# Kernel tuning notes

Measured on AMD Instinct MI355X. Metric: run time of the kernel, lower is better.

## Reference

```python
import jax, jax.numpy as jnp
import numpy as np
from jax import lax

B, T, M = 32, 1024, 40
CONV, H, C = 128, 256, 10
EPS = 1e-5
POOLS = (5, 4, 2)  # mel-axis maxpool sizes; 5*4*2 == n_mels == 40


def setup_inputs() -> dict:
    key = jax.random.key(0)
    ks = jax.random.split(key, 30)
    rn = lambda k, s, sc=0.05: jax.random.normal(k, s, dtype=jnp.float32) * sc
    inp = {}
    inp["features"] = jax.random.normal(ks[0], (B, 1, T, M), dtype=jnp.float32)
    inp["targets"] = (jax.random.uniform(ks[1], (B, T, C)) > 0.5).astype(jnp.float32)
    inp["force_mask"] = jax.random.bernoulli(ks[2], 0.7, (T, B))  # teacher_forcing_prob=0.7
    chans = [(1, CONV), (CONV, CONV), (CONV, CONV)]
    for i, (ci, co) in enumerate(chans, 1):
        inp[f"W{i}"] = rn(ks[3 * i], (co, ci, 5, 5))
        inp[f"b{i}"] = jnp.zeros((co,), jnp.float32)
        inp[f"g{i}"] = jnp.ones((co,), jnp.float32)
        inp[f"be{i}"] = jnp.zeros((co,), jnp.float32)
        inp[f"m{i}"] = rn(ks[3 * i + 1], (co,), 0.01)
        inp[f"v{i}"] = jnp.ones((co,), jnp.float32)
    inp["Wih"] = rn(ks[20], (3 * H, CONV + C))
    inp["Whh"] = rn(ks[21], (3 * H, H))
    inp["bih"] = jnp.zeros((3 * H,), jnp.float32)
    inp["bhh"] = jnp.zeros((3 * H,), jnp.float32)
    inp["Wf"] = rn(ks[22], (C, H))
    inp["bf"] = jnp.zeros((C,), jnp.float32)
    return inp


def _conv_block(x, W, b, g, be, m, v, pool):
    # Conv2d(k=5, s=1, p=2) + BatchNorm2d (inference) + ReLU + MaxPool2d((1,pool))
    y = lax.conv_general_dilated(x, W, window_strides=(1, 1), padding=((2, 2), (2, 2)),
                                 dimension_numbers=("NCHW", "OIHW", "NCHW"))
    y = y + b[None, :, None, None]
    scale = g * lax.rsqrt(v + EPS)
    y = y * scale[None, :, None, None] + (be - m * scale)[None, :, None, None]
    y = jax.nn.relu(y)
    return lax.reduce_window(y, -jnp.inf, lax.max, (1, 1, 1, pool), (1, 1, 1, pool), "VALID")


def _crnn(features, targets, force_mask, W1, b1, g1, be1, m1, v1, W2, b2, g2, be2, m2, v2,
          W3, b3, g3, be3, m3, v3, Wih, Whh, bih, bhh, Wf, bf):
    x = features  # [B,1,T,M]
    for (W, b, g, be, m, v, p) in ((W1, b1, g1, be1, m1, v1, POOLS[0]),
                                   (W2, b2, g2, be2, m2, v2, POOLS[1]),
                                   (W3, b3, g3, be3, m3, v3, POOLS[2])):
        x = _conv_block(x, W, b, g, be, m, v, p)
    feats = jnp.transpose(x[:, :, :, 0], (2, 0, 1))  # mel pooled to 1 -> [T,B,CONV]

    def step(carry, xs):
        h, tf = carry
        xt, tgt_t, ft = xs  # [B,CONV], [B,C], [B]
        inp = jnp.concatenate([xt, tf], axis=-1)  # [B, CONV+C]
        gi = inp @ Wih.T + bih
        gh = h @ Whh.T + bhh
        ir, iz, inn = jnp.split(gi, 3, axis=-1)
        hr, hz, hn = jnp.split(gh, 3, axis=-1)
        r = jax.nn.sigmoid(ir + hr)
        z = jax.nn.sigmoid(iz + hz)
        n = jnp.tanh(inn + r * hn)
        h = (1.0 - z) * n + z * h
        out = h @ Wf.T + bf  # [B,C]
        pred = (jax.nn.sigmoid(out) > 0.5).astype(jnp.float32)
        tf = jnp.where(ft[:, None], tgt_t, pred)  # teacher-forcing select
        return (h, tf), out

    init = (jnp.zeros((B, H), jnp.float32), jnp.zeros((B, C), jnp.float32))
    xs = (feats, jnp.transpose(targets, (1, 0, 2)), force_mask)
    _, outs = lax.scan(step, init, xs)  # [T,B,C]
    return jnp.transpose(outs, (1, 0, 2))  # [B,T,C]


def reference(features, targets, force_mask, W1, b1, g1, be1, m1, v1, W2, b2, g2, be2, m2, v2,
              W3, b3, g3, be3, m3, v3, Wih, Whh, bih, bhh, Wf, bf):
    return _crnn(features, targets, force_mask, W1, b1, g1, be1, m1, v1, W2, b2, g2, be2, m2, v2,
                 W3, b3, g3, be3, m3, v3, Wih, Whh, bih, bhh, Wf, bf)
```

## Files before the change

kernel.cpp:

```cpp
#include <hip/hip_runtime.h>
#include <math.h>

#define EPSF 1e-5f

typedef __attribute__((ext_vector_type(2))) float f2;
typedef __attribute__((ext_vector_type(4))) float f4;
typedef __attribute__((ext_vector_type(8))) _Float16 f16x8;

template<int CTRL>
__device__ __forceinline__ float dpp_add(float v) {
    int s = __builtin_amdgcn_update_dpp(0, __float_as_int(v), CTRL, 0xf, 0xf, true);
    return v + __int_as_float(s);
}

#define HQ(d) ((d) + (((d) >> 4) << 2))

__global__ __launch_bounds__(256) void k_prep(
    const float* __restrict__ Wih, const float* __restrict__ Whh,
    const float* __restrict__ W2, const float* __restrict__ W3,
    const unsigned char* __restrict__ fmask,
    unsigned int* __restrict__ WhhP, float* __restrict__ WxT,
    _Float16* __restrict__ W2F, float* __restrict__ W3T, int* __restrict__ flag)
{
    int idx = blockIdx.x * 256 + threadIdx.x;
    if (idx < 98304) {
        int T = idx >> 8;
        int lane = (idx >> 2) & 63;
        int j = idx & 3;
        int RT = T >> 3, kt = T & 7;
        int row = RT * 16 + (lane & 15);
        int col = kt * 32 + (lane >> 4) * 8 + j * 2;
        union { _Float16 h[2]; unsigned int u; } pk;
        pk.h[0] = (_Float16)Whh[row * 256 + col];
        pk.h[1] = (_Float16)Whh[row * 256 + col + 1];
        WhhP[idx] = pk.u;
    }
    if (idx < 105984) {
        int j = idx / 138, k = idx % 138;
        if (k < 128) WxT[k * 768 + j] = Wih[idx];
    }
    if (idx < 409600) {
        int f = idx & 7, lane = (idx >> 3) & 63, cot = (idx >> 9) & 7;
        int cc = (idx >> 12) & 3, T = idx >> 14;
        int k = cc * 32 + (lane >> 4) * 8 + f;
        int co = cot * 16 + (lane & 15);
        int dt = T / 5, dm = T % 5;
        W2F[idx] = (_Float16)W2[co * 3200 + k * 25 + dt * 5 + dm];
        int co3 = idx / 3200, r = idx % 3200;
        int ci = r / 25, tap = r % 25;
        W3T[(tap * 128 + ci) * 128 + co3] = W3[idx];
    }
    if (idx == 0) {
        int nz = 0;
        for (int i = 0; i < 4096; i++) if ((i & 3) != 0) nz |= fmask[i];
        *flag = nz ? 0 : 1;
    }
}

__global__ __launch_bounds__(256) void k_conv1(
    const float* __restrict__ X, const float* __restrict__ W1,
    const float* __restrict__ bb, const float* __restrict__ gg,
    const float* __restrict__ be, const float* __restrict__ mm_,
    const float* __restrict__ vv, _Float16* __restrict__ X1h,
    _Float16* __restrict__ X1l)
{
    __shared__ __align__(16) float xs[8][44];
    __shared__ __align__(16) float ws[25][128];
    __shared__ float sc[128], sh[128];
    int bid = blockIdx.x;
    int b = bid >> 8, t0 = (bid & 255) << 2;
    int tid = threadIdx.x;
    for (int e = tid; e < 8 * 44; e += 256) {
        int tt = e / 44, mm = e % 44;
        int gt = t0 + tt - 2, gm = mm - 2;
        float val = 0.f;
        if (gt >= 0 && gt < 1024 && gm >= 0 && gm < 40)
            val = X[(b * 1024 + gt) * 40 + gm];
        xs[tt][mm] = val;
    }
    for (int e = tid; e < 3200; e += 256) {
        int tap = e >> 7, co = e & 127;
        ws[tap][co] = W1[co * 25 + tap];
    }
    if (tid < 128) {
        float s = gg[tid] / sqrtf(vv[tid] + EPSF);
        sc[tid] = s;
        sh[tid] = (bb[tid] - mm_[tid]) * s + be[tid];
    }
    __syncthreads();
    int cog = tid >> 5;
    int m1i = (tid >> 2) & 7;
    int tp  = tid & 3;
    int co0 = cog * 16;
    float val[5][16];
#pragma unroll
    for (int p = 0; p < 5; p++)
#pragma unroll
        for (int i = 0; i < 16; i++) val[p][i] = 0.f;
#pragma unroll
    for (int dt = 0; dt < 5; dt++) {
#pragma unroll
        for (int dm = 0; dm < 5; dm++) {
            float w[16];
#pragma unroll
            for (int i = 0; i < 16; i += 4)
                *(float4*)&w[i] = *(const float4*)&ws[dt * 5 + dm][co0 + i];
#pragma unroll
            for (int p = 0; p < 5; p++) {
                float x = xs[tp + dt][m1i * 5 + p + dm];
#pragma unroll
                for (int i = 0; i < 16; i++) val[p][i] = fmaf(x, w[i], val[p][i]);
            }
        }
    }
    f16x8 h0, h1, l0, l1;
#pragma unroll
    for (int i = 0; i < 16; i++) {
        float s = sc[co0 + i], h = sh[co0 + i];
        float mx = 0.f;
#pragma unroll
        for (int p = 0; p < 5; p++) {
            float y = fmaf(val[p][i], s, h);
            y = fmaxf(y, 0.f);
            mx = fmaxf(mx, y);
        }
        _Float16 hh = (_Float16)mx;
        _Float16 ll = (_Float16)(mx - (float)hh);
        if (i < 8) { h0[i] = hh; l0[i] = ll; }
        else       { h1[i - 8] = hh; l1[i - 8] = ll; }
    }
    long off = (((long)(b * 1024 + t0 + tp)) * 8 + m1i) * 128 + co0;
    *(f16x8*)&X1h[off] = h0;
    *(f16x8*)&X1h[off + 8] = h1;
    *(f16x8*)&X1l[off] = l0;
    *(f16x8*)&X1l[off + 8] = l1;
}

__global__ __launch_bounds__(256) void k_conv2(
    const _Float16* __restrict__ X1h, const _Float16* __restrict__ X1l,
    const _Float16* __restrict__ W2F,
    const float* __restrict__ bb, const float* __restrict__ gg,
    const float* __restrict__ be, const float* __restrict__ mm_,
    const float* __restrict__ vv, float* __restrict__ X2)
{
    __shared__ __align__(16) _Float16 xsh[144 * 40];
    __shared__ __align__(16) _Float16 xsl[144 * 40];
    __shared__ float sc[128], sh[128];
    int bid = blockIdx.x;
    int b = bid >> 7, t0 = (bid & 127) << 3;
    int tid = threadIdx.x;
    int wv = tid >> 6, l = tid & 63;
    int rowc = l & 15, ks = (l >> 4) << 3;
    int tloc = rowc >> 3, mloc = rowc & 7;
    if (tid < 128) {
        float s = gg[tid] / sqrtf(vv[tid] + EPSF);
        sc[tid] = s;
        sh[tid] = (bb[tid] - mm_[tid]) * s + be[tid];
    }
    f4 acc[4][2];
#pragma unroll
    for (int Mt = 0; Mt < 4; Mt++) {
        acc[Mt][0] = (f4){0.f, 0.f, 0.f, 0.f};
        acc[Mt][1] = (f4){0.f, 0.f, 0.f, 0.f};
    }

    for (int cc = 0; cc < 4; cc++) {
        __syncthreads();
        for (int e = tid; e < 1152; e += 256) {
            int w2 = (e >= 576) ? 1 : 0;
            int ee = e - 576 * w2;
            int r = ee >> 2, q = ee & 3;
            int tt = r / 12, mm2 = r % 12;
            int gt = t0 + tt - 2, gm = mm2 - 2;
            f16x8 v;
#pragma unroll
            for (int z = 0; z < 8; z++) v[z] = (_Float16)0.f;
            if (gt >= 0 && gt < 1024 && gm >= 0 && gm < 8) {
                const _Float16* src = w2 ? X1l : X1h;
                v = *(const f16x8*)&src[(((long)(b * 1024 + gt)) * 8 + gm) * 128 + cc * 32 + q * 8];
            }
            _Float16* dst = w2 ? xsl : xsh;
            *(f16x8*)&dst[r * 40 + q * 8] = v;
        }
        __syncthreads();
        for (int dt = 0; dt < 5; dt++) {
#pragma unroll
            for (int dm = 0; dm < 5; dm++) {
                const _Float16* wb = &W2F[(((long)((dt * 5 + dm) * 4 + cc) * 8) * 64) * 8];
                f16x8 b0 = *(const f16x8*)&wb[((wv * 2 + 0) * 64 + l) * 8];
                f16x8 b1 = *(const f16x8*)&wb[((wv * 2 + 1) * 64 + l) * 8];
#pragma unroll
                for (int Mt = 0; Mt < 4; Mt++) {
                    int ai = ((Mt * 2 + tloc + dt) * 12 + (mloc + dm)) * 40 + ks;
                    f16x8 ah = *(const f16x8*)&xsh[ai];
                    f16x8 al = *(const f16x8*)&xsl[ai];
                    acc[Mt][0] = __builtin_amdgcn_mfma_f32_16x16x32_f16(ah, b0, acc[Mt][0], 0, 0, 0);
                    acc[Mt][0] = __builtin_amdgcn_mfma_f32_16x16x32_f16(al, b0, acc[Mt][0], 0, 0, 0);
                    acc[Mt][1] = __builtin_amdgcn_mfma_f32_16x16x32_f16(ah, b1, acc[Mt][1], 0, 0, 0);
                    acc[Mt][1] = __builtin_amdgcn_mfma_f32_16x16x32_f16(al, b1, acc[Mt][1], 0, 0, 0);
                }
            }
        }
    }
    int g = l >> 4;
    int tof = g >> 1, m2 = g & 1;
#pragma unroll
    for (int Mt = 0; Mt < 4; Mt++) {
        int t = t0 + Mt * 2 + tof;
#pragma unroll
        for (int c2 = 0; c2 < 2; c2++) {
            int co = (wv * 2 + c2) * 16 + rowc;
            float s = sc[co], h = sh[co];
            f4 av = acc[Mt][c2];
            float mx = 0.f;
#pragma unroll
            for (int j = 0; j < 4; j++) {
                float y = fmaf(av[j], s, h);
                y = fmaxf(y, 0.f);
                mx = fmaxf(mx, y);
            }
            X2[(((long)(b * 1024 + t)) * 2 + m2) * 128 + co] = mx;
        }
    }
}

__global__ __launch_bounds__(256) void k_conv3(
    const float* __restrict__ X2, const float* __restrict__ W3T,
    const float* __restrict__ bb, const float* __restrict__ gg,
    const float* __restrict__ be, const float* __restrict__ mm_,
    const float* __restrict__ vv, float* __restrict__ F)
{
    __shared__ __align__(16) float xs[68 * 66];
    __shared__ __align__(16) float ws[3][32][64];
    __shared__ float sc[64], sh[64];
    int bid = blockIdx.x;
    int coh = bid & 1, t0 = ((bid >> 1) & 15) << 6, b = bid >> 5;
    int co_base = coh * 64;
    int tid = threadIdx.x;
    int tp = tid & 15, cog = tid >> 4;
    if (tid < 64) {
        int co = co_base + tid;
        float s = gg[co] / sqrtf(vv[co] + EPSF);
        sc[tid] = s;
        sh[tid] = (bb[co] - mm_[co]) * s + be[co];
    }
    float acc[4][4][2];
#pragma unroll
    for (int tc = 0; tc < 4; tc++)
#pragma unroll
        for (int c = 0; c < 4; c++) { acc[tc][c][0] = 0.f; acc[tc][c][1] = 0.f; }

    for (int cc = 0; cc < 4; cc++) {
        __syncthreads();
        for (int e = tid; e < 68 * 64; e += 256) {
            int tt = e >> 6, r = e & 63;
            int ci = r >> 1, m = r & 1;
            int gt = t0 + tt - 2;
            float v = 0.f;
            if (gt >= 0 && gt < 1024)
                v = X2[(((long)(b * 1024 + gt)) * 2 + m) * 128 + cc * 32 + ci];
            xs[tt * 66 + ci * 2 + m] = v;
        }
        for (int dt = 0; dt < 5; dt++) {
            __syncthreads();
            for (int e = tid; e < 3 * 32 * 64; e += 256) {
                int co = e & 63, ci = (e >> 6) & 31, dmi = e >> 11;
                ws[dmi][ci][co] = W3T[((dt * 5 + dmi + 1) * 128 + cc * 32 + ci) * 128 + co_base + co];
            }
            __syncthreads();
            for (int ci = 0; ci < 32; ci++) {
                float w1[4], w2[4], w3[4];
                *(float4*)w1 = *(const float4*)&ws[0][ci][cog * 4];
                *(float4*)w2 = *(const float4*)&ws[1][ci][cog * 4];
                *(float4*)w3 = *(const float4*)&ws[2][ci][cog * 4];
#pragma unroll
                for (int tc = 0; tc < 4; tc++) {
                    float2 x = *(const float2*)&xs[(tc * 16 + tp + dt) * 66 + ci * 2];
#pragma unroll
                    for (int c = 0; c < 4; c++) acc[tc][c][0] = fmaf(w2[c], x.x, acc[tc][c][0]);
#pragma unroll
                    for (int c = 0; c < 4; c++) acc[tc][c][0] = fmaf(w3[c], x.y, acc[tc][c][0]);
#pragma unroll
                    for (int c = 0; c < 4; c++) acc[tc][c][1] = fmaf(w1[c], x.x, acc[tc][c][1]);
#pragma unroll
                    for (int c = 0; c < 4; c++) acc[tc][c][1] = fmaf(w2[c], x.y, acc[tc][c][1]);
                }
            }
        }
    }
#pragma unroll
    for (int tc = 0; tc < 4; tc++) {
        float4 ov;
        float* po = (float*)&ov;
#pragma unroll
        for (int c = 0; c < 4; c++) {
            float s = sc[cog * 4 + c], h = sh[cog * 4 + c];
            float y0 = fmaxf(fmaf(acc[tc][c][0], s, h), 0.f);
            float y1 = fmaxf(fmaf(acc[tc][c][1], s, h), 0.f);
            po[c] = fmaxf(y0, y1);
        }
        *(float4*)&F[((long)(t0 + tc * 16 + tp) * 32 + b) * 128 + co_base + cog * 4] = ov;
    }
}

__global__ __launch_bounds__(256) void k_gemm(
    const float* __restrict__ F, const float* __restrict__ WxT,
    const float* __restrict__ bih, float* __restrict__ Gx)
{
    __shared__ __align__(16) float Fs[64][33];
    __shared__ __align__(16) float Ws[32][256];
    int bid = blockIdx.x;
    int jt = bid % 3, tb0 = (bid / 3) * 64;
    int tid = threadIdx.x;
    int tx = tid & 31, ty = tid >> 5;
    float acc[8][8];
#pragma unroll
    for (int i = 0; i < 8; i++)
#pragma unroll
        for (int j = 0; j < 8; j++) acc[i][j] = 0.f;
    for (int cc = 0; cc < 4; cc++) {
        __syncthreads();
        for (int e = tid; e < 64 * 32; e += 256) {
            int ci = e & 31, i = e >> 5;
            Fs[i][ci] = F[(long)(tb0 + i) * 128 + cc * 32 + ci];
        }
        for (int e = tid; e < 32 * 256; e += 256) {
            int jj = e & 255, ci = e >> 8;
            Ws[ci][jj] = WxT[(cc * 32 + ci) * 768 + jt * 256 + jj];
        }
        __syncthreads();
        for (int ci = 0; ci < 32; ci++) {
            float a[8], w[8];
#pragma unroll
            for (int i = 0; i < 8; i++) a[i] = Fs[ty * 8 + i][ci];
            *(float4*)&w[0] = *(const float4*)&Ws[ci][tx * 8];
            *(float4*)&w[4] = *(const float4*)&Ws[ci][tx * 8 + 4];
#pragma unroll
            for (int i = 0; i < 8; i++)
#pragma unroll
                for (int j = 0; j < 8; j++) acc[i][j] = fmaf(a[i], w[j], acc[i][j]);
        }
    }
    float bj[8];
#pragma unroll
    for (int j = 0; j < 8; j++) bj[j] = bih[jt * 256 + tx * 8 + j];
#pragma unroll
    for (int i = 0; i < 8; i++) {
        float o[8];
#pragma unroll
        for (int j = 0; j < 8; j++) o[j] = acc[i][j] + bj[j];
        float* dst = &Gx[(long)(tb0 + ty * 8 + i) * 768 + jt * 256 + tx * 8];
        *(float4*)&dst[0] = *(float4*)&o[0];
        *(float4*)&dst[4] = *(float4*)&o[4];
    }
}

__global__ __attribute__((amdgpu_waves_per_eu(2, 2))) __launch_bounds__(512) void k_gru2(
    const f16x8* __restrict__ Wp8, const float* __restrict__ Gx,
    const float* __restrict__ Wih, const float* __restrict__ bhh_g,
    const float* __restrict__ Wf, const float* __restrict__ bf_g,
    const float* __restrict__ targets, const unsigned char* __restrict__ fmask,
    const int* __restrict__ flag, float* __restrict__ out)
{
    __shared__ __align__(16) float hq[320];
    __shared__ __align__(16) _Float16 hqh[256];
    __shared__ __align__(16) _Float16 hqh2[256];
    __shared__ __align__(16) float gsum[768];
    __shared__ float tfl[16];
    __shared__ float bhL[768];
    __shared__ __align__(16) float wtfL[7680];
    __shared__ __align__(16) float WfL[3200];
    const int b = blockIdx.x, tid = threadIdx.x;
    const int wv = tid >> 6, l = tid & 63;
    const int kg = l >> 4;
    const int cl = l & 15;
    const bool isGate = (tid < 256);
    const bool isProj = (tid >= 256 && tid < 416);
    const int oc = (tid - 256) >> 4, seg = tid & 15;
    const bool isWr = isProj && (seg == 15);

    f16x8 wq[48];
    {
        const f16x8* wp = Wp8 + (long)(wv * 48) * 64 + l;
#pragma unroll
        for (int q = 0; q < 48; q++) wq[q] = wp[q * 64];
    }
#pragma unroll
    for (int q = 0; q < 48; q++) asm volatile("" : "+v"(wq[q]));

    for (int e = tid; e < 7680; e += 512) {
        int cp = e >> 8, jj = e & 255;
        int gg = cp / 10, c = cp - gg * 10;
        wtfL[e] = Wih[(gg * 256 + jj) * 138 + 128 + c];
    }
    for (int e = tid; e < 3200; e += 512) {
        int oo = e / 320, rem = e - oo * 320;
        int sg = rem / 20, ii = rem - sg * 20;
        WfL[e] = (ii < 16) ? Wf[oo * 256 + sg * 16 + ii] : 0.f;
    }
    for (int e = tid; e < 768; e += 512) { bhL[e] = bhh_g[e]; gsum[e] = 0.f; }
    if (tid < 320) hq[tid] = 0.f;
    if (tid < 256) { hqh[tid] = (_Float16)0.f; hqh2[tid] = (_Float16)0.f; }
    if (tid < 16) tfl[tid] = 0.f;
    float bfc = isProj ? bf_g[oc] : 0.f;
    const int int32mode = flag[0];
    float hold = 0.f;
    const _Float16* bsrc = (cl == 1) ? hqh2 : hqh;
    __syncthreads();

    for (int t = 0; t < 1024; t++) {
        float gxr = 0.f, gxz = 0.f, gxn = 0.f;
        if (isGate) {
            const float* gx = &Gx[((long)t * 32 + b) * 768];
            gxr = gx[tid]; gxz = gx[tid + 256]; gxn = gx[tid + 512];
        }
        float tgt = 0.f; int fmv = 0;
        if (isWr) {
            tgt = targets[((long)b * 1024 + t) * 10 + oc];
            fmv = int32mode ? ((const int*)fmask)[t * 32 + b] : (int)fmask[t * 32 + b];
        }

        f4 acc[6];
#pragma unroll
        for (int rt = 0; rt < 6; rt++) acc[rt] = (f4){0.f, 0.f, 0.f, 0.f};
#pragma unroll
        for (int kt = 0; kt < 8; kt++) {
            f16x8 bv = *(const f16x8*)&bsrc[kt * 32 + kg * 8];
#pragma unroll
            for (int rt = 0; rt < 6; rt++)
                acc[rt] = __builtin_amdgcn_mfma_f32_16x16x32_f16(
                    wq[rt * 8 + kt], bv, acc[rt], 0, 0, 0);
        }
#pragma unroll
        for (int rt = 0; rt < 6; rt++) {
#pragma unroll
            for (int c = 0; c < 4; c++) acc[rt][c] = dpp_add<0x111>(acc[rt][c]);
        }
        if (cl == 1) {
#pragma unroll
            for (int rt = 0; rt < 6; rt++)
                *(f4*)&gsum[(wv * 6 + rt) * 16 + kg * 4] = acc[rt];
        }
        __syncthreads();

        if (isGate) {
            float gr = gxr, gz = gxz, gn = gxn;
#pragma unroll
            for (int c = 0; c < 10; c++) {
                float tv = tfl[c];
                gr = fmaf(tv, wtfL[c * 256 + tid], gr);
                gz = fmaf(tv, wtfL[(10 + c) * 256 + tid], gz);
                gn = fmaf(tv, wtfL[(20 + c) * 256 + tid], gn);
            }
            float ar = gsum[tid] + bhL[tid];
            float az = gsum[tid + 256] + bhL[tid + 256];
            float an = gsum[tid + 512] + bhL[tid + 512];
            float r = 1.0f / (1.0f + expf(-(gr + ar)));
            float z = 1.0f / (1.0f + expf(-(gz + az)));
            float n = tanhf(fmaf(r, an, gn));
            float hnew = (1.0f - z) * n + z * hold;
            hold = hnew;
            _Float16 hh = (_Float16)hnew;
            hq[HQ(tid)] = hnew;
            hqh[tid] = hh;
            hqh2[tid] = (_Float16)(hnew - (float)hh);
        }
        __syncthreads();

        if (isProj) {
            float s = 0.f;
#pragma unroll
            for (int qq = 0; qq < 4; qq++) {
                f4 h4 = *(const f4*)&hq[seg * 20 + qq * 4];
                f4 wvv = *(const f4*)&WfL[oc * 320 + seg * 20 + qq * 4];
                s = fmaf(wvv.x, h4.x, s);
                s = fmaf(wvv.y, h4.y, s);
                s = fmaf(wvv.z, h4.z, s);
                s = fmaf(wvv.w, h4.w, s);
            }
            s = dpp_add<0x111>(s);
            s = dpp_add<0x112>(s);
            s = dpp_add<0x114>(s);
            s = dpp_add<0x118>(s);
            if (isWr) {
                float o = s + bfc;
                out[((long)b * 1024 + t) * 10 + oc] = o;
                float pred = (o > 0.f) ? 1.f : 0.f;
                tfl[oc] = fmv ? tgt : pred;
            }
        }
    }
}

extern "C" void kernel_launch(void* const* d_in, const int* in_sizes, int n_in,
                              void* d_out, int out_size, void* d_ws, size_t ws_size,
                              hipStream_t stream) {
    (void)in_sizes; (void)n_in; (void)out_size; (void)ws_size;
    const float* features = (const float*)d_in[0];
    const float* targets  = (const float*)d_in[1];
    const unsigned char* fmask = (const unsigned char*)d_in[2];
    const float* W1  = (const float*)d_in[3];
    const float* b1  = (const float*)d_in[4];
    const float* g1  = (const float*)d_in[5];
    const float* be1 = (const float*)d_in[6];
    const float* m1  = (const float*)d_in[7];
    const float* v1  = (const float*)d_in[8];
    const float* W2  = (const float*)d_in[9];
    const float* b2  = (const float*)d_in[10];
    const float* g2  = (const float*)d_in[11];
    const float* be2 = (const float*)d_in[12];
    const float* m2  = (const float*)d_in[13];
    const float* v2  = (const float*)d_in[14];
    const float* W3  = (const float*)d_in[15];
    const float* b3  = (const float*)d_in[16];
    const float* g3  = (const float*)d_in[17];
    const float* be3 = (const float*)d_in[18];
    const float* m3  = (const float*)d_in[19];
    const float* v3  = (const float*)d_in[20];
    const float* Wih = (const float*)d_in[21];
    const float* Whh = (const float*)d_in[22];
    const float* bih = (const float*)d_in[23];
    const float* bhh = (const float*)d_in[24];
    const float* Wf  = (const float*)d_in[25];
    const float* bf  = (const float*)d_in[26];

    char* w = (char*)d_ws;
    unsigned int* WhhP = (unsigned int*)(w + 0);
    float* WxT = (float*)(w + 786432);
    _Float16* W2F = (_Float16*)(w + 1179648);
    float* W3T = (float*)(w + 2818048);
    int*   flag = (int*)(w + 4456448);
    _Float16* X1h = (_Float16*)(w + 4456960);
    _Float16* X1l = (_Float16*)(w + 4456960 + 67108864);
    float* Gx  = (float*)(w + 4456960);
    float* X2  = (float*)(w + 4456960 + 134217728);
    float* F   = (float*)(w + 4456960 + 134217728 + 33554432);
    float* out = (float*)d_out;

    k_prep<<<1600, 256, 0, stream>>>(Wih, Whh, W2, W3, fmask, WhhP, WxT, W2F, W3T, flag);
    k_conv1<<<8192, 256, 0, stream>>>(features, W1, b1, g1, be1, m1, v1, X1h, X1l);
    k_conv2<<<4096, 256, 0, stream>>>(X1h, X1l, W2F, b2, g2, be2, m2, v2, X2);
    k_conv3<<<1024, 256, 0, stream>>>(X2, W3T, b3, g3, be3, m3, v3, F);
    k_gemm<<<1536, 256, 0, stream>>>(F, WxT, bih, Gx);
    k_gru2<<<32, 512, 0, stream>>>((const f16x8*)WhhP, Gx, Wih, bhh, Wf, bf,
                                   targets, fmask, flag, out);
}
```

Before: 3.616 ms.

## Split GRU recurrent weights across registers, LDS and global reloads; fold biases

The GRU kernel used to hold all 48 fp16 weight fragments per lane in registers. It now keeps 12 in registers, stages 15 in dynamic LDS and re-reads the rest from global (cache) on every timestep, so register pressure drops. The r/z recurrent biases are folded into the input GEMM bias, and the teacher-forcing input weights are stored as fp16 in LDS to save space. The catch is extra LDS and global traffic on every serial timestep of the latency-bound recurrence, plus a small loss of precision in the teacher-forcing weights.

```diff
diff --git a/kernel.cpp b/kernel.cpp
--- a/kernel.cpp
+++ b/kernel.cpp
@@ -305,7 +305,8 @@
 
 __global__ __launch_bounds__(256) void k_gemm(
     const float* __restrict__ F, const float* __restrict__ WxT,
-    const float* __restrict__ bih, float* __restrict__ Gx)
+    const float* __restrict__ bih, const float* __restrict__ bhh,
+    float* __restrict__ Gx)
 {
     __shared__ __align__(16) float Fs[64][33];
     __shared__ __align__(16) float Ws[32][256];
@@ -343,7 +344,10 @@
     }
     float bj[8];
 #pragma unroll
-    for (int j = 0; j < 8; j++) bj[j] = bih[jt * 256 + tx * 8 + j];
+    for (int j = 0; j < 8; j++) {
+        int col = jt * 256 + tx * 8 + j;
+        bj[j] = bih[col] + (col < 512 ? bhh[col] : 0.f);
+    }
 #pragma unroll
     for (int i = 0; i < 8; i++) {
         float o[8];
@@ -362,13 +366,13 @@
     const float* __restrict__ targets, const unsigned char* __restrict__ fmask,
     const int* __restrict__ flag, float* __restrict__ out)
 {
+    extern __shared__ __align__(16) _Float16 dynw[];
     __shared__ __align__(16) float hq[320];
     __shared__ __align__(16) _Float16 hqh[256];
     __shared__ __align__(16) _Float16 hqh2[256];
     __shared__ __align__(16) float gsum[768];
     __shared__ float tfl[16];
-    __shared__ float bhL[768];
-    __shared__ __align__(16) float wtfL[7680];
+    __shared__ __align__(16) _Float16 wtfL[7680];
     __shared__ __align__(16) float WfL[3200];
     const int b = blockIdx.x, tid = threadIdx.x;
     const int wv = tid >> 6, l = tid & 63;
@@ -378,31 +382,35 @@
     const bool isProj = (tid >= 256 && tid < 416);
     const int oc = (tid - 256) >> 4, seg = tid & 15;
     const bool isWr = isProj && (seg == 15);
-
-    f16x8 wq[48];
-    {
-        const f16x8* wp = Wp8 + (long)(wv * 48) * 64 + l;
-#pragma unroll
-        for (int q = 0; q < 48; q++) wq[q] = wp[q * 64];
-    }
-#pragma unroll
-    for (int q = 0; q < 48; q++) asm volatile("" : "+v"(wq[q]));
+    f16x8* wlds = (f16x8*)dynw;
+
+    const f16x8* wp = Wp8 + (long)(wv * 48) * 64 + l;
+
+    f16x8 wq[12];
+#pragma unroll
+    for (int q = 0; q < 12; q++) wq[q] = wp[q * 64];
+#pragma unroll
+    for (int q = 0; q < 12; q++) asm volatile("" : "+v"(wq[q]));
+
+#pragma unroll
+    for (int fi = 0; fi < 15; fi++) wlds[fi * 512 + tid] = wp[(12 + fi) * 64];
 
     for (int e = tid; e < 7680; e += 512) {
         int cp = e >> 8, jj = e & 255;
         int gg = cp / 10, c = cp - gg * 10;
-        wtfL[e] = Wih[(gg * 256 + jj) * 138 + 128 + c];
+        wtfL[e] = (_Float16)Wih[(gg * 256 + jj) * 138 + 128 + c];
     }
     for (int e = tid; e < 3200; e += 512) {
         int oo = e / 320, rem = e - oo * 320;
         int sg = rem / 20, ii = rem - sg * 20;
         WfL[e] = (ii < 16) ? Wf[oo * 256 + sg * 16 + ii] : 0.f;
     }
-    for (int e = tid; e < 768; e += 512) { bhL[e] = bhh_g[e]; gsum[e] = 0.f; }
+    for (int e = tid; e < 768; e += 512) gsum[e] = 0.f;
     if (tid < 320) hq[tid] = 0.f;
     if (tid < 256) { hqh[tid] = (_Float16)0.f; hqh2[tid] = (_Float16)0.f; }
     if (tid < 16) tfl[tid] = 0.f;
     float bfc = isProj ? bf_g[oc] : 0.f;
+    float bh2 = isGate ? bhh_g[tid + 512] : 0.f;
     const int int32mode = flag[0];
     float hold = 0.f;
     const _Float16* bsrc = (cl == 1) ? hqh2 : hqh;
@@ -425,11 +433,23 @@
         for (int rt = 0; rt < 6; rt++) acc[rt] = (f4){0.f, 0.f, 0.f, 0.f};
 #pragma unroll
         for (int kt = 0; kt < 8; kt++) {
+            f16x8 s4 = wp[(32 + kt) * 64];
+            f16x8 s5 = wp[(40 + kt) * 64];
+            f16x8 s3;
+            if (kt >= 3) s3 = wp[(24 + kt) * 64];
             f16x8 bv = *(const f16x8*)&bsrc[kt * 32 + kg * 8];
-#pragma unroll
-            for (int rt = 0; rt < 6; rt++)
-                acc[rt] = __builtin_amdgcn_mfma_f32_16x16x32_f16(
-                    wq[rt * 8 + kt], bv, acc[rt], 0, 0, 0);
+            acc[0] = __builtin_amdgcn_mfma_f32_16x16x32_f16(wq[kt], bv, acc[0], 0, 0, 0);
+            if (kt < 4)
+                acc[1] = __builtin_amdgcn_mfma_f32_16x16x32_f16(wq[8 + kt], bv, acc[1], 0, 0, 0);
+            else
+                acc[1] = __builtin_amdgcn_mfma_f32_16x16x32_f16(wlds[(kt - 4) * 512 + tid], bv, acc[1], 0, 0, 0);
+            acc[2] = __builtin_amdgcn_mfma_f32_16x16x32_f16(wlds[(4 + kt) * 512 + tid], bv, acc[2], 0, 0, 0);
+            if (kt < 3)
+                acc[3] = __builtin_amdgcn_mfma_f32_16x16x32_f16(wlds[(12 + kt) * 512 + tid], bv, acc[3], 0, 0, 0);
+            else
+                acc[3] = __builtin_amdgcn_mfma_f32_16x16x32_f16(s3, bv, acc[3], 0, 0, 0);
+            acc[4] = __builtin_amdgcn_mfma_f32_16x16x32_f16(s4, bv, acc[4], 0, 0, 0);
+            acc[5] = __builtin_amdgcn_mfma_f32_16x16x32_f16(s5, bv, acc[5], 0, 0, 0);
         }
 #pragma unroll
         for (int rt = 0; rt < 6; rt++) {
@@ -448,13 +468,13 @@
 #pragma unroll
             for (int c = 0; c < 10; c++) {
                 float tv = tfl[c];
-                gr = fmaf(tv, wtfL[c * 256 + tid], gr);
-                gz = fmaf(tv, wtfL[(10 + c) * 256 + tid], gz);
-                gn = fmaf(tv, wtfL[(20 + c) * 256 + tid], gn);
-            }
-            float ar = gsum[tid] + bhL[tid];
-            float az = gsum[tid + 256] + bhL[tid + 256];
-            float an = gsum[tid + 512] + bhL[tid + 512];
+                gr = fmaf(tv, (float)wtfL[c * 256 + tid], gr);
+                gz = fmaf(tv, (float)wtfL[(10 + c) * 256 + tid], gz);
+                gn = fmaf(tv, (float)wtfL[(20 + c) * 256 + tid], gn);
+            }
+            float ar = gsum[tid];
+            float az = gsum[tid + 256];
+            float an = gsum[tid + 512] + bh2;
             float r = 1.0f / (1.0f + expf(-(gr + ar)));
             float z = 1.0f / (1.0f + expf(-(gz + az)));
             float n = tanhf(fmaf(r, an, gn));
@@ -537,11 +557,15 @@
     float* F   = (float*)(w + 4456960 + 134217728 + 33554432);
     float* out = (float*)d_out;
 
+    const int GRU_DYN_LDS = 15 * 512 * 16;
+    (void)hipFuncSetAttribute((const void*)k_gru2,
+        hipFuncAttributeMaxDynamicSharedMemorySize, GRU_DYN_LDS);
+
     k_prep<<<1600, 256, 0, stream>>>(Wih, Whh, W2, W3, fmask, WhhP, WxT, W2F, W3T, flag);
     k_conv1<<<8192, 256, 0, stream>>>(features, W1, b1, g1, be1, m1, v1, X1h, X1l);
     k_conv2<<<4096, 256, 0, stream>>>(X1h, X1l, W2F, b2, g2, be2, m2, v2, X2);
     k_conv3<<<1024, 256, 0, stream>>>(X2, W3T, b3, g3, be3, m3, v3, F);
-    k_gemm<<<1536, 256, 0, stream>>>(F, WxT, bih, Gx);
-    k_gru2<<<32, 512, 0, stream>>>((const f16x8*)WhhP, Gx, Wih, bhh, Wf, bf,
-                                   targets, fmask, flag, out);
-}
+    k_gemm<<<1536, 256, 0, stream>>>(F, WxT, bih, bhh, Gx);
+    k_gru2<<<32, 512, GRU_DYN_LDS, stream>>>((const f16x8*)WhhP, Gx, Wih, bhh, Wf, bf,
+                                             targets, fmask, flag, out);
+}
```

Result: faster. 3.351 ms (-7.3%).
